# Performance work log

Measured on AMD Instinct MI355X. Metric: run time of the kernel, lower is better.

Reference implementation:

```python
import jax, jax.numpy as jnp
import numpy as np

S, B, H = 512, 32, 1024      # seq, batch, hidden_size
L = 4096                      # total spans (flattened ragged labels)
D = 1024                      # label_size (feature dim)
V = 32000                     # vocab size


def setup_inputs() -> dict:
    key = jax.random.key(0)
    ks = jax.random.split(key, 10)
    hidden = jax.random.normal(ks[0], (S, B, H), dtype=jnp.float32)
    span_bid = jax.random.randint(ks[1], (L,), 0, B)
    span_begin = jax.random.randint(ks[2], (L,), 0, S)
    span_end_m1 = jax.random.randint(ks[3], (L,), 0, S)  # (end - 1) index
    tags = jax.random.randint(ks[4], (L,), 0, V)
    # hidden2feature: Linear(2H -> D) with bias, Tanh
    W1 = jax.random.normal(ks[5], (D, 2 * H), dtype=jnp.float32) * (1.0 / np.sqrt(2 * H))
    b1 = jnp.zeros((D,), dtype=jnp.float32)
    # SoftmaxLoss h2o: Linear(D -> V, bias=False)
    Wout = jax.random.normal(ks[6], (V, D), dtype=jnp.float32) * (1.0 / np.sqrt(D))
    # discard probs from synthetic frequency counts
    counts = jax.random.uniform(ks[7], (V,), minval=1e-5, maxval=1.0)
    freqs = counts / counts.sum()
    discard_probs = jnp.clip(1.0 - jnp.sqrt(1e-4 / freqs), 0.0, None)
    return {"hidden": hidden, "W1": W1, "b1": b1, "Wout": Wout,
            "discard_probs": discard_probs, "span_bid": span_bid,
            "span_begin": span_begin, "span_end_m1": span_end_m1, "tags": tags}


def reference(hidden, W1, b1, Wout, discard_probs, span_bid, span_begin, span_end_m1, tags):
    # gather span endpoint embeddings: [L, H] each
    emb_b = hidden[span_begin, span_bid]
    emb_e = hidden[span_end_m1, span_bid]
    span_emb = jnp.concatenate([emb_b, emb_e], axis=-1)          # [L, 2H]
    feat = jnp.tanh(span_emb @ W1.T + b1)                        # [L, D]
    logits = feat @ Wout.T                                       # [L, V]
    logp = jax.nn.log_softmax(logits, axis=-1)
    nll = -jnp.take_along_axis(logp, tags[:, None], axis=-1)[:, 0]  # [L]
    scaled = 1.0 - discard_probs[tags]
    n_tags = tags.shape[0]
    return jnp.sum(nll * scaled) / (n_tags + 1e-5)
```

## Files before the change

kernel.cpp:

```cpp
#include <hip/hip_runtime.h>
#include <hip/hip_bf16.h>

#define LSPANS 4096
#define BB 32
#define HH 1024
#define DD 1024
#define VV 32000
#define K1 2048
#define NT2 250

typedef unsigned short u16;
typedef __attribute__((ext_vector_type(8))) short bf16x8v;
typedef __attribute__((ext_vector_type(4))) float f32x4v;

__device__ __forceinline__ u16 f2bf(float x) {
  union { float f; unsigned u; } v; v.f = x;
  unsigned r = (v.u >> 16) & 1u;
  return (u16)((v.u + 0x7fffu + r) >> 16);
}

__global__ void cvt_kernel(const float* __restrict__ in, u16* __restrict__ out, int n4) {
  int i = blockIdx.x * blockDim.x + threadIdx.x;
  int stride = gridDim.x * blockDim.x;
  for (; i < n4; i += stride) {
    float4 v = ((const float4*)in)[i];
    ushort4 o;
    o.x = f2bf(v.x); o.y = f2bf(v.y); o.z = f2bf(v.z); o.w = f2bf(v.w);
    ((ushort4*)out)[i] = o;
  }
}

__global__ void gather_kernel(const float* __restrict__ hidden,
                              const int* __restrict__ bid,
                              const int* __restrict__ sb,
                              const int* __restrict__ se,
                              u16* __restrict__ out) {
  int l = blockIdx.x;
  int t = threadIdx.x;
  int b  = bid[l];
  const float* p0 = hidden + ((size_t)sb[l] * BB + b) * HH;
  const float* p1 = hidden + ((size_t)se[l] * BB + b) * HH;
  u16* dst = out + (size_t)l * K1;
  float4 v0 = ((const float4*)p0)[t];
  float4 v1 = ((const float4*)p1)[t];
  ushort4 o0; o0.x = f2bf(v0.x); o0.y = f2bf(v0.y); o0.z = f2bf(v0.z); o0.w = f2bf(v0.w);
  ushort4 o1; o1.x = f2bf(v1.x); o1.y = f2bf(v1.y); o1.z = f2bf(v1.z); o1.w = f2bf(v1.w);
  ((ushort4*)dst)[t]          = o0;
  ((ushort4*)(dst + HH))[t]   = o1;
}

template <int K_, int EPI>
__launch_bounds__(256, 2)
__global__ void gemm_kernel(const u16* __restrict__ A, const u16* __restrict__ B,
                            int Ntot,
                            const float* __restrict__ bias, u16* __restrict__ feat_out,
                            const int* __restrict__ tags,
                            float* __restrict__ pmax, float* __restrict__ psum,
                            float* __restrict__ ltag) {
  __shared__ __align__(16) u16 As[128 * 64];
  __shared__ __align__(16) u16 Bs[128 * 64];
  __shared__ float rmax[2][128];
  __shared__ float rsum[2][128];
  __shared__ int   stags[128];

  const int tid  = threadIdx.x;
  const int lane = tid & 63;
  const int w    = tid >> 6;
  const int wm   = w & 1;
  const int wn   = w >> 1;
  const int q    = lane >> 4;
  const int lm   = lane & 15;
  const int mBase = blockIdx.x * 128;
  const int nBase = blockIdx.y * 128;

  if (EPI == 2 && tid < 128) stags[tid] = tags[mBase + tid];

  f32x4v acc[4][4];
#pragma unroll
  for (int i = 0; i < 4; ++i)
#pragma unroll
    for (int j = 0; j < 4; ++j) acc[i][j] = (f32x4v){0.f, 0.f, 0.f, 0.f};

  const int srow = w * 32 + (lane >> 3);
  const int scol = ((lane & 7) ^ (lane >> 3)) * 8;
  const u16* Ag = A + (size_t)(mBase + srow) * K_ + scol;
  const u16* Bg = B + (size_t)(nBase + srow) * K_ + scol;

  for (int k0 = 0; k0 < K_; k0 += 64) {
#pragma unroll
    for (int c = 0; c < 4; ++c) {
      __builtin_amdgcn_global_load_lds(
          (const __attribute__((address_space(1))) void*)(Ag + k0 + (size_t)c * 8 * K_),
          (__attribute__((address_space(3))) void*)(As + (w * 32 + c * 8) * 64), 16, 0, 0);
    }
#pragma unroll
    for (int c = 0; c < 4; ++c) {
      __builtin_amdgcn_global_load_lds(
          (const __attribute__((address_space(1))) void*)(Bg + k0 + (size_t)c * 8 * K_),
          (__attribute__((address_space(3))) void*)(Bs + (w * 32 + c * 8) * 64), 16, 0, 0);
    }
    __syncthreads();
#pragma unroll
    for (int kk = 0; kk < 64; kk += 32) {
      bf16x8v af[4], bfr[4];
      const int sw = lm & 7;
#pragma unroll
      for (int i = 0; i < 4; ++i) {
        int row = wm * 64 + i * 16 + lm;
        int kch = (kk >> 3) + q;
        af[i] = *(const bf16x8v*)(As + row * 64 + ((kch ^ sw) << 3));
      }
#pragma unroll
      for (int j = 0; j < 4; ++j) {
        int row = wn * 64 + j * 16 + lm;
        int kch = (kk >> 3) + q;
        bfr[j] = *(const bf16x8v*)(Bs + row * 64 + ((kch ^ sw) << 3));
      }
#pragma unroll
      for (int i = 0; i < 4; ++i)
#pragma unroll
        for (int j = 0; j < 4; ++j)
          acc[i][j] = __builtin_amdgcn_mfma_f32_16x16x32_bf16(af[i], bfr[j], acc[i][j], 0, 0, 0);
    }
    __syncthreads();
  }

  if constexpr (EPI == 1) {
    float bj[4];
#pragma unroll
    for (int j = 0; j < 4; ++j) bj[j] = bias[nBase + wn * 64 + j * 16 + lm];
#pragma unroll
    for (int i = 0; i < 4; ++i)
#pragma unroll
      for (int j = 0; j < 4; ++j)
#pragma unroll
        for (int r = 0; r < 4; ++r) {
          int tr = wm * 64 + i * 16 + q * 4 + r;
          int tc = wn * 64 + j * 16 + lm;
          float v = tanhf(acc[i][j][r] + bj[j]);
          feat_out[(size_t)(mBase + tr) * Ntot + nBase + tc] = f2bf(v);
        }
  }

  if constexpr (EPI == 2) {
#pragma unroll
    for (int i = 0; i < 4; ++i)
#pragma unroll
      for (int r = 0; r < 4; ++r) {
        float m = fmaxf(fmaxf(acc[i][0][r], acc[i][1][r]),
                        fmaxf(acc[i][2][r], acc[i][3][r]));
#pragma unroll
        for (int off = 1; off < 16; off <<= 1) m = fmaxf(m, __shfl_xor(m, off, 64));
        if (lm == 0) rmax[wn][wm * 64 + i * 16 + q * 4 + r] = m;
      }
    __syncthreads();
#pragma unroll
    for (int i = 0; i < 4; ++i)
#pragma unroll
      for (int r = 0; r < 4; ++r) {
        int tr = wm * 64 + i * 16 + q * 4 + r;
        float M = fmaxf(rmax[0][tr], rmax[1][tr]);
        float s = __expf(acc[i][0][r] - M) + __expf(acc[i][1][r] - M) +
                  __expf(acc[i][2][r] - M) + __expf(acc[i][3][r] - M);
#pragma unroll
        for (int off = 1; off < 16; off <<= 1) s += __shfl_xor(s, off, 64);
        if (lm == 0) rsum[wn][tr] = s;
      }
    __syncthreads();
    if (tid < 128) {
      float M = fmaxf(rmax[0][tid], rmax[1][tid]);
      float S = rsum[0][tid] + rsum[1][tid];
      pmax[(size_t)blockIdx.y * LSPANS + mBase + tid] = M;
      psum[(size_t)blockIdx.y * LSPANS + mBase + tid] = S;
    }
#pragma unroll
    for (int i = 0; i < 4; ++i)
#pragma unroll
      for (int r = 0; r < 4; ++r) {
        int tr = wm * 64 + i * 16 + q * 4 + r;
        int tg = stags[tr];
#pragma unroll
        for (int j = 0; j < 4; ++j) {
          int gc = nBase + wn * 64 + j * 16 + lm;
          if (tg == gc) ltag[mBase + tr] = acc[i][j][r];
        }
      }
  }
}

__global__ void finalize_kernel(const float* __restrict__ pmax, const float* __restrict__ psum,
                                const float* __restrict__ ltag, const int* __restrict__ tags,
                                const float* __restrict__ dprob, float* __restrict__ out) {
  int l = blockIdx.x * blockDim.x + threadIdx.x;
  const float* pm = pmax + l;
  const float* ps = psum + l;
  float M = -1e30f;
  for (int t = 0; t < NT2; ++t) M = fmaxf(M, pm[(size_t)t * LSPANS]);
  float S = 0.f;
  for (int t = 0; t < NT2; ++t) S += ps[(size_t)t * LSPANS] * __expf(pm[(size_t)t * LSPANS] - M);
  float nll = M + logf(S) - ltag[l];
  float wgt = 1.0f - dprob[tags[l]];
  float val = nll * wgt * (1.0f / (4096.0f + 1e-5f));
  __shared__ float red[4];
#pragma unroll
  for (int off = 32; off; off >>= 1) val += __shfl_down(val, off, 64);
  if ((threadIdx.x & 63) == 0) red[threadIdx.x >> 6] = val;
  __syncthreads();
  if (threadIdx.x == 0) atomicAdd(out, red[0] + red[1] + red[2] + red[3]);
}

extern "C" void kernel_launch(void* const* d_in, const int* in_sizes, int n_in,
                              void* d_out, int out_size, void* d_ws, size_t ws_size,
                              hipStream_t stream) {
  const float* hidden = (const float*)d_in[0];
  const float* W1     = (const float*)d_in[1];
  const float* b1     = (const float*)d_in[2];
  const float* Wout   = (const float*)d_in[3];
  const float* dprob  = (const float*)d_in[4];
  const int*   bid    = (const int*)d_in[5];
  const int*   sb     = (const int*)d_in[6];
  const int*   se     = (const int*)d_in[7];
  const int*   tags   = (const int*)d_in[8];
  float* out = (float*)d_out;

  char* ws = (char*)d_ws;
  u16* A1    = (u16*)ws;                 ws += (size_t)LSPANS * K1 * 2;
  u16* W1b   = (u16*)ws;                 ws += (size_t)DD * K1 * 2;
  u16* Woutb = (u16*)ws;                 ws += (size_t)VV * DD * 2;
  u16* feat  = (u16*)ws;                 ws += (size_t)LSPANS * DD * 2;
  float* pmax = (float*)ws;              ws += (size_t)NT2 * LSPANS * 4;
  float* psum = (float*)ws;              ws += (size_t)NT2 * LSPANS * 4;
  float* ltag = (float*)ws;              ws += (size_t)LSPANS * 4;

  hipMemsetAsync(d_out, 0, sizeof(float), stream);

  {
    int n4 = DD * K1 / 4;
    cvt_kernel<<<(n4 + 255) / 256, 256, 0, stream>>>(W1, W1b, n4);
  }
  {
    int n4 = VV * DD / 4;
    cvt_kernel<<<(n4 + 255) / 256, 256, 0, stream>>>(Wout, Woutb, n4);
  }
  gather_kernel<<<LSPANS, 256, 0, stream>>>(hidden, bid, sb, se, A1);

  gemm_kernel<K1, 1><<<dim3(LSPANS / 128, DD / 128), 256, 0, stream>>>(
      A1, W1b, DD, b1, feat, nullptr, nullptr, nullptr, nullptr);

  gemm_kernel<DD, 2><<<dim3(LSPANS / 128, NT2), 256, 0, stream>>>(
      feat, Woutb, VV, nullptr, nullptr, tags, pmax, psum, ltag);

  finalize_kernel<<<LSPANS / 256, 256, 0, stream>>>(pmax, psum, ltag, tags, dprob, out);
}
```

Baseline: 653.0 us.

## Run vocab projection GEMM in FP8 with scaled MFMA

Converts Wout and the tanh features to FP8 (e4m3) and replaces the bf16 MFMA in the vocab-logit GEMM with the 16x16x128 scaled f8f6f4 MFMA using unit scales. The K tile is widened to 128 bytes per row, with a matching swizzle and LDS layout. This halves the operand bytes and doubles the math rate per instruction for the dominant GEMM, and also shrinks the Wout conversion writes. The cost is lower precision in the logits, which may move the loss outside tolerance.

```diff
diff --git a/kernel.cpp b/kernel.cpp
--- a/kernel.cpp
+++ b/kernel.cpp
@@ -10,13 +10,24 @@
 #define NT2 250
 
 typedef unsigned short u16;
+typedef unsigned char u8;
 typedef __attribute__((ext_vector_type(8))) short bf16x8v;
 typedef __attribute__((ext_vector_type(4))) float f32x4v;
+typedef __attribute__((ext_vector_type(8))) int i32x8v;
+typedef __attribute__((ext_vector_type(4))) int i32x4v;
+
+#define SCALE1 0x7F7F7F7F
 
 __device__ __forceinline__ u16 f2bf(float x) {
   union { float f; unsigned u; } v; v.f = x;
   unsigned r = (v.u >> 16) & 1u;
   return (u16)((v.u + 0x7fffu + r) >> 16);
+}
+
+__device__ __forceinline__ int pk4_fp8(float a, float b, float c, float d) {
+  int p = __builtin_amdgcn_cvt_pk_fp8_f32(a, b, 0, false);
+  p = __builtin_amdgcn_cvt_pk_fp8_f32(c, d, p, true);
+  return p;
 }
 
 __global__ void cvt_kernel(const float* __restrict__ in, u16* __restrict__ out, int n4) {
@@ -27,6 +38,15 @@
     ushort4 o;
     o.x = f2bf(v.x); o.y = f2bf(v.y); o.z = f2bf(v.z); o.w = f2bf(v.w);
     ((ushort4*)out)[i] = o;
+  }
+}
+
+__global__ void cvt_fp8_kernel(const float* __restrict__ in, int* __restrict__ out, int n4) {
+  int i = blockIdx.x * blockDim.x + threadIdx.x;
+  int stride = gridDim.x * blockDim.x;
+  for (; i < n4; i += stride) {
+    float4 v = ((const float4*)in)[i];
+    out[i] = pk4_fp8(v.x, v.y, v.z, v.w);
   }
 }
 
@@ -49,19 +69,11 @@
   ((ushort4*)(dst + HH))[t]   = o1;
 }
 
-template <int K_, int EPI>
 __launch_bounds__(256, 2)
-__global__ void gemm_kernel(const u16* __restrict__ A, const u16* __restrict__ B,
-                            int Ntot,
-                            const float* __restrict__ bias, u16* __restrict__ feat_out,
-                            const int* __restrict__ tags,
-                            float* __restrict__ pmax, float* __restrict__ psum,
-                            float* __restrict__ ltag) {
+__global__ void gemm1_kernel(const u16* __restrict__ A, const u16* __restrict__ B,
+                             const float* __restrict__ bias, u8* __restrict__ feat_out) {
   __shared__ __align__(16) u16 As[128 * 64];
   __shared__ __align__(16) u16 Bs[128 * 64];
-  __shared__ float rmax[2][128];
-  __shared__ float rsum[2][128];
-  __shared__ int   stags[128];
 
   const int tid  = threadIdx.x;
   const int lane = tid & 63;
@@ -73,8 +85,6 @@
   const int mBase = blockIdx.x * 128;
   const int nBase = blockIdx.y * 128;
 
-  if (EPI == 2 && tid < 128) stags[tid] = tags[mBase + tid];
-
   f32x4v acc[4][4];
 #pragma unroll
   for (int i = 0; i < 4; ++i)
@@ -83,20 +93,20 @@
 
   const int srow = w * 32 + (lane >> 3);
   const int scol = ((lane & 7) ^ (lane >> 3)) * 8;
-  const u16* Ag = A + (size_t)(mBase + srow) * K_ + scol;
-  const u16* Bg = B + (size_t)(nBase + srow) * K_ + scol;
-
-  for (int k0 = 0; k0 < K_; k0 += 64) {
+  const u16* Ag = A + (size_t)(mBase + srow) * K1 + scol;
+  const u16* Bg = B + (size_t)(nBase + srow) * K1 + scol;
+
+  for (int k0 = 0; k0 < K1; k0 += 64) {
 #pragma unroll
     for (int c = 0; c < 4; ++c) {
       __builtin_amdgcn_global_load_lds(
-          (const __attribute__((address_space(1))) void*)(Ag + k0 + (size_t)c * 8 * K_),
+          (const __attribute__((address_space(1))) void*)(Ag + k0 + (size_t)c * 8 * K1),
           (__attribute__((address_space(3))) void*)(As + (w * 32 + c * 8) * 64), 16, 0, 0);
     }
 #pragma unroll
     for (int c = 0; c < 4; ++c) {
       __builtin_amdgcn_global_load_lds(
-          (const __attribute__((address_space(1))) void*)(Bg + k0 + (size_t)c * 8 * K_),
+          (const __attribute__((address_space(1))) void*)(Bg + k0 + (size_t)c * 8 * K1),
           (__attribute__((address_space(3))) void*)(Bs + (w * 32 + c * 8) * 64), 16, 0, 0);
     }
     __syncthreads();
@@ -125,67 +135,141 @@
     __syncthreads();
   }
 
-  if constexpr (EPI == 1) {
-    float bj[4];
-#pragma unroll
-    for (int j = 0; j < 4; ++j) bj[j] = bias[nBase + wn * 64 + j * 16 + lm];
-#pragma unroll
-    for (int i = 0; i < 4; ++i)
-#pragma unroll
-      for (int j = 0; j < 4; ++j)
-#pragma unroll
-        for (int r = 0; r < 4; ++r) {
-          int tr = wm * 64 + i * 16 + q * 4 + r;
-          int tc = wn * 64 + j * 16 + lm;
-          float v = tanhf(acc[i][j][r] + bj[j]);
-          feat_out[(size_t)(mBase + tr) * Ntot + nBase + tc] = f2bf(v);
-        }
-  }
-
-  if constexpr (EPI == 2) {
-#pragma unroll
-    for (int i = 0; i < 4; ++i)
-#pragma unroll
-      for (int r = 0; r < 4; ++r) {
-        float m = fmaxf(fmaxf(acc[i][0][r], acc[i][1][r]),
-                        fmaxf(acc[i][2][r], acc[i][3][r]));
-#pragma unroll
-        for (int off = 1; off < 16; off <<= 1) m = fmaxf(m, __shfl_xor(m, off, 64));
-        if (lm == 0) rmax[wn][wm * 64 + i * 16 + q * 4 + r] = m;
-      }
-    __syncthreads();
-#pragma unroll
-    for (int i = 0; i < 4; ++i)
+  float bj[4];
+#pragma unroll
+  for (int j = 0; j < 4; ++j) bj[j] = bias[nBase + wn * 64 + j * 16 + lm];
+#pragma unroll
+  for (int i = 0; i < 4; ++i)
+#pragma unroll
+    for (int j = 0; j < 4; ++j)
 #pragma unroll
       for (int r = 0; r < 4; ++r) {
         int tr = wm * 64 + i * 16 + q * 4 + r;
-        float M = fmaxf(rmax[0][tr], rmax[1][tr]);
-        float s = __expf(acc[i][0][r] - M) + __expf(acc[i][1][r] - M) +
-                  __expf(acc[i][2][r] - M) + __expf(acc[i][3][r] - M);
-#pragma unroll
-        for (int off = 1; off < 16; off <<= 1) s += __shfl_xor(s, off, 64);
-        if (lm == 0) rsum[wn][tr] = s;
+        int tc = wn * 64 + j * 16 + lm;
+        float v = tanhf(acc[i][j][r] + bj[j]);
+        int p = __builtin_amdgcn_cvt_pk_fp8_f32(v, v, 0, false);
+        feat_out[(size_t)(mBase + tr) * DD + nBase + tc] = (u8)(p & 0xff);
       }
+}
+
+__launch_bounds__(256, 2)
+__global__ void gemm2_kernel(const u8* __restrict__ A, const u8* __restrict__ B,
+                             const int* __restrict__ tags,
+                             float* __restrict__ pmax, float* __restrict__ psum,
+                             float* __restrict__ ltag) {
+  __shared__ __align__(16) u8 As[128 * 128];
+  __shared__ __align__(16) u8 Bs[128 * 128];
+  __shared__ float rmax[2][128];
+  __shared__ float rsum[2][128];
+  __shared__ int   stags[128];
+
+  const int tid  = threadIdx.x;
+  const int lane = tid & 63;
+  const int w    = tid >> 6;
+  const int wm   = w & 1;
+  const int wn   = w >> 1;
+  const int q    = lane >> 4;
+  const int lm   = lane & 15;
+  const int mBase = blockIdx.x * 128;
+  const int nBase = blockIdx.y * 128;
+
+  if (tid < 128) stags[tid] = tags[mBase + tid];
+
+  f32x4v acc[4][4];
+#pragma unroll
+  for (int i = 0; i < 4; ++i)
+#pragma unroll
+    for (int j = 0; j < 4; ++j) acc[i][j] = (f32x4v){0.f, 0.f, 0.f, 0.f};
+
+  const int srow = w * 32 + (lane >> 3);
+  const int scol = ((lane & 7) ^ (lane >> 3)) * 16;
+  const u8* Ag = A + (size_t)(mBase + srow) * DD + scol;
+  const u8* Bg = B + (size_t)(nBase + srow) * DD + scol;
+
+  for (int k0 = 0; k0 < DD; k0 += 128) {
+#pragma unroll
+    for (int c = 0; c < 4; ++c) {
+      __builtin_amdgcn_global_load_lds(
+          (const __attribute__((address_space(1))) void*)(Ag + k0 + (size_t)c * 8 * DD),
+          (__attribute__((address_space(3))) void*)(As + (w * 32 + c * 8) * 128), 16, 0, 0);
+    }
+#pragma unroll
+    for (int c = 0; c < 4; ++c) {
+      __builtin_amdgcn_global_load_lds(
+          (const __attribute__((address_space(1))) void*)(Bg + k0 + (size_t)c * 8 * DD),
+          (__attribute__((address_space(3))) void*)(Bs + (w * 32 + c * 8) * 128), 16, 0, 0);
+    }
     __syncthreads();
-    if (tid < 128) {
-      float M = fmaxf(rmax[0][tid], rmax[1][tid]);
-      float S = rsum[0][tid] + rsum[1][tid];
-      pmax[(size_t)blockIdx.y * LSPANS + mBase + tid] = M;
-      psum[(size_t)blockIdx.y * LSPANS + mBase + tid] = S;
+
+    i32x8v af[4], bfr[4];
+    const int sw = lm & 7;
+    const int c0 = ((2 * q) ^ sw) * 16;
+    const int c1 = ((2 * q + 1) ^ sw) * 16;
+#pragma unroll
+    for (int i = 0; i < 4; ++i) {
+      int row = wm * 64 + i * 16 + lm;
+      i32x4v lo = *(const i32x4v*)(As + row * 128 + c0);
+      i32x4v hi = *(const i32x4v*)(As + row * 128 + c1);
+      af[i] = (i32x8v){lo[0], lo[1], lo[2], lo[3], hi[0], hi[1], hi[2], hi[3]};
+    }
+#pragma unroll
+    for (int j = 0; j < 4; ++j) {
+      int row = wn * 64 + j * 16 + lm;
+      i32x4v lo = *(const i32x4v*)(Bs + row * 128 + c0);
+      i32x4v hi = *(const i32x4v*)(Bs + row * 128 + c1);
+      bfr[j] = (i32x8v){lo[0], lo[1], lo[2], lo[3], hi[0], hi[1], hi[2], hi[3]};
     }
 #pragma unroll
     for (int i = 0; i < 4; ++i)
 #pragma unroll
-      for (int r = 0; r < 4; ++r) {
-        int tr = wm * 64 + i * 16 + q * 4 + r;
-        int tg = stags[tr];
-#pragma unroll
-        for (int j = 0; j < 4; ++j) {
-          int gc = nBase + wn * 64 + j * 16 + lm;
-          if (tg == gc) ltag[mBase + tr] = acc[i][j][r];
-        }
+      for (int j = 0; j < 4; ++j)
+        acc[i][j] = __builtin_amdgcn_mfma_scale_f32_16x16x128_f8f6f4(
+            af[i], bfr[j], acc[i][j], 0, 0, 0, SCALE1, 0, SCALE1);
+    __syncthreads();
+  }
+
+#pragma unroll
+  for (int i = 0; i < 4; ++i)
+#pragma unroll
+    for (int r = 0; r < 4; ++r) {
+      float m = fmaxf(fmaxf(acc[i][0][r], acc[i][1][r]),
+                      fmaxf(acc[i][2][r], acc[i][3][r]));
+#pragma unroll
+      for (int off = 1; off < 16; off <<= 1) m = fmaxf(m, __shfl_xor(m, off, 64));
+      if (lm == 0) rmax[wn][wm * 64 + i * 16 + q * 4 + r] = m;
+    }
+  __syncthreads();
+#pragma unroll
+  for (int i = 0; i < 4; ++i)
+#pragma unroll
+    for (int r = 0; r < 4; ++r) {
+      int tr = wm * 64 + i * 16 + q * 4 + r;
+      float M = fmaxf(rmax[0][tr], rmax[1][tr]);
+      float s = __expf(acc[i][0][r] - M) + __expf(acc[i][1][r] - M) +
+                __expf(acc[i][2][r] - M) + __expf(acc[i][3][r] - M);
+#pragma unroll
+      for (int off = 1; off < 16; off <<= 1) s += __shfl_xor(s, off, 64);
+      if (lm == 0) rsum[wn][tr] = s;
+    }
+  __syncthreads();
+  if (tid < 128) {
+    float M = fmaxf(rmax[0][tid], rmax[1][tid]);
+    float S = rsum[0][tid] + rsum[1][tid];
+    pmax[(size_t)blockIdx.y * LSPANS + mBase + tid] = M;
+    psum[(size_t)blockIdx.y * LSPANS + mBase + tid] = S;
+  }
+#pragma unroll
+  for (int i = 0; i < 4; ++i)
+#pragma unroll
+    for (int r = 0; r < 4; ++r) {
+      int tr = wm * 64 + i * 16 + q * 4 + r;
+      int tg = stags[tr];
+#pragma unroll
+      for (int j = 0; j < 4; ++j) {
+        int gc = nBase + wn * 64 + j * 16 + lm;
+        if (tg == gc) ltag[mBase + tr] = acc[i][j][r];
       }
-  }
+    }
 }
 
 __global__ void finalize_kernel(const float* __restrict__ pmax, const float* __restrict__ psum,
@@ -224,10 +308,10 @@
   float* out = (float*)d_out;
 
   char* ws = (char*)d_ws;
-  u16* A1    = (u16*)ws;                 ws += (size_t)LSPANS * K1 * 2;
-  u16* W1b   = (u16*)ws;                 ws += (size_t)DD * K1 * 2;
-  u16* Woutb = (u16*)ws;                 ws += (size_t)VV * DD * 2;
-  u16* feat  = (u16*)ws;                 ws += (size_t)LSPANS * DD * 2;
+  u16* A1     = (u16*)ws;                ws += (size_t)LSPANS * K1 * 2;
+  u16* W1b    = (u16*)ws;                ws += (size_t)DD * K1 * 2;
+  u8*  Wout8  = (u8*)ws;                 ws += (size_t)VV * DD;
+  u8*  feat8  = (u8*)ws;                 ws += (size_t)LSPANS * DD;
   float* pmax = (float*)ws;              ws += (size_t)NT2 * LSPANS * 4;
   float* psum = (float*)ws;              ws += (size_t)NT2 * LSPANS * 4;
   float* ltag = (float*)ws;              ws += (size_t)LSPANS * 4;
@@ -240,15 +324,13 @@
   }
   {
     int n4 = VV * DD / 4;
-    cvt_kernel<<<(n4 + 255) / 256, 256, 0, stream>>>(Wout, Woutb, n4);
+    cvt_fp8_kernel<<<(n4 + 255) / 256, 256, 0, stream>>>(Wout, (int*)Wout8, n4);
   }
   gather_kernel<<<LSPANS, 256, 0, stream>>>(hidden, bid, sb, se, A1);
 
-  gemm_kernel<K1, 1><<<dim3(LSPANS / 128, DD / 128), 256, 0, stream>>>(
-      A1, W1b, DD, b1, feat, nullptr, nullptr, nullptr, nullptr);
-
-  gemm_kernel<DD, 2><<<dim3(LSPANS / 128, NT2), 256, 0, stream>>>(
-      feat, Woutb, VV, nullptr, nullptr, tags, pmax, psum, ltag);
+  gemm1_kernel<<<dim3(LSPANS / 128, DD / 128), 256, 0, stream>>>(A1, W1b, b1, feat8);
+
+  gemm2_kernel<<<dim3(LSPANS / 128, NT2), 256, 0, stream>>>(feat8, Wout8, tags, pmax, psum, ltag);
 
   finalize_kernel<<<LSPANS / 256, 256, 0, stream>>>(pmax, psum, ltag, tags, dprob, out);
 }
```

After: 1.178 ms. 1.8x slower.
